# Performance work log

Hardware: AMD Instinct MI355X
Metric: run time of the kernel (lower is better)

## Reference

```python
import jax, jax.numpy as jnp
import numpy as np

K = 3

def setup_inputs() -> dict:
    key = jax.random.key(0)
    k1, k2, k3, k4 = jax.random.split(key, 4)
    B, N, F_in, T, F_out = 8, 2048, 16, 12, 32
    x = jax.random.normal(k1, (B, N, F_in, T), dtype=jnp.float32)
    spatial_attention = jax.random.uniform(k2, (B, N, N), dtype=jnp.float32)
    node_embeddings = jax.random.normal(k3, (N, 16), dtype=jnp.float32)
    theta = jax.random.normal(k4, (K, F_in, F_out), dtype=jnp.float32) * 0.1
    return {"x": x, "spatial_attention": spatial_attention,
            "node_embeddings": node_embeddings, "theta": theta}

def _cheb_polys(node_embeddings, N, K):
    # supports = softmax(relu(E E^T), axis=1)
    supports = jax.nn.softmax(jax.nn.relu(node_embeddings @ node_embeddings.T), axis=1)
    polys = [jnp.eye(N, dtype=supports.dtype), supports]
    for _ in range(2, K):
        polys.append(2.0 * supports @ polys[-1] - polys[-2])
    return jnp.stack(polys[:K], axis=0)  # (K, N, N)

def reference(x, spatial_attention, node_embeddings, theta):
    B, N, F_in, T = x.shape
    polys = _cheb_polys(node_embeddings, N, K)             # (K,N,N)
    # T_k_with_at = polys[k] * attention (broadcast over batch);
    # rhs = T_k_with_at^T @ graph_signal for every timestep:
    # (K,N,N)*(B,N,N) contracted with (B,N,F,T) over source node n -> (K,B,M,F,T)
    rhs = jnp.einsum('knm,bnm,bnft->kbmft', polys, spatial_attention, x)
    # accumulate rhs @ theta_k over k -> (B,M,F_out,T)
    out = jnp.einsum('kbmft,kfo->bmot', rhs, theta)
    return jax.nn.relu(out)
```

## Files before the change

kernel.cpp:

```cpp
#include <hip/hip_runtime.h>

#define NN    2048
#define BATCH 8
#define FIN   16
#define TT    12
#define FOUT  32
#define FT    (FIN*TT)
#define OT    (FOUT*TT)

typedef unsigned short ushort_t;
typedef __attribute__((ext_vector_type(8))) short   short8;
typedef __attribute__((ext_vector_type(4))) float   f32x4;
typedef __attribute__((ext_vector_type(4))) unsigned short us4;
typedef __attribute__((ext_vector_type(8))) unsigned short us8;

__device__ __forceinline__ float b2f(unsigned short u) {
    union { unsigned int i; float f; } v; v.i = ((unsigned int)u) << 16; return v.f;
}
__device__ __forceinline__ unsigned short f2b(float f) {
    union { float f; unsigned int i; } v; v.f = f;
    unsigned int x = v.i;
    x += 0x7fffu + ((x >> 16) & 1u);
    return (unsigned short)(x >> 16);
}

#define LGKM0()   asm volatile("s_waitcnt lgkmcnt(0)" ::: "memory")
#define BARRIER() __builtin_amdgcn_s_barrier()

__global__ __launch_bounds__(256)
void k_supports(const float* __restrict__ E, ushort_t* __restrict__ Sb) {
    const int n = blockIdx.x;
    __shared__ float row[NN];
    __shared__ float red[256];
    const int tid = threadIdx.x;

    const f32x4 en0 = *(const f32x4*)&E[n * 16 + 0];
    const f32x4 en1 = *(const f32x4*)&E[n * 16 + 4];
    const f32x4 en2 = *(const f32x4*)&E[n * 16 + 8];
    const f32x4 en3 = *(const f32x4*)&E[n * 16 + 12];

    float lmax = 0.0f;
    for (int m = tid; m < NN; m += 256) {
        const f32x4* Em = (const f32x4*)&E[(size_t)m * 16];
        const f32x4 e0 = Em[0], e1 = Em[1], e2 = Em[2], e3 = Em[3];
        float d = 0.0f;
        #pragma unroll
        for (int j = 0; j < 4; ++j) d += en0[j] * e0[j];
        #pragma unroll
        for (int j = 0; j < 4; ++j) d += en1[j] * e1[j];
        #pragma unroll
        for (int j = 0; j < 4; ++j) d += en2[j] * e2[j];
        #pragma unroll
        for (int j = 0; j < 4; ++j) d += en3[j] * e3[j];
        d = fmaxf(d, 0.0f);
        row[m] = d;
        lmax = fmaxf(lmax, d);
    }
    red[tid] = lmax; __syncthreads();
    for (int s = 128; s > 0; s >>= 1) {
        if (tid < s) red[tid] = fmaxf(red[tid], red[tid + s]);
        __syncthreads();
    }
    const float mx = red[0];
    __syncthreads();

    float lsum = 0.0f;
    for (int m = tid; m < NN; m += 256) {
        float e = __expf(row[m] - mx);
        row[m] = e;
        lsum += e;
    }
    red[tid] = lsum; __syncthreads();
    for (int s = 128; s > 0; s >>= 1) {
        if (tid < s) red[tid] += red[tid + s];
        __syncthreads();
    }
    const float inv = 1.0f / red[0];
    for (int m = tid; m < NN; m += 256) Sb[(size_t)n * NN + m] = f2b(row[m] * inv);
}

__global__ __launch_bounds__(256)
void k_pack_st(const ushort_t* __restrict__ Sb, ushort_t* __restrict__ SbT) {
    const int r0 = blockIdx.x * 64, c0 = blockIdx.y * 64;
    __shared__ ushort_t Lt[64][65];
    const int tid = threadIdx.x;
    #pragma unroll
    for (int p = 0; p < 2; ++p) {
        const int i = (tid >> 3) + p * 32;
        const int j8 = (tid & 7) * 8;
        us8 v = *(const us8*)&Sb[(size_t)(r0 + i) * NN + c0 + j8];
        #pragma unroll
        for (int e = 0; e < 8; ++e) Lt[i][j8 + e] = v[e];
    }
    __syncthreads();
    #pragma unroll
    for (int p = 0; p < 2; ++p) {
        const int jj = (tid >> 3) + p * 32;
        const int i8 = (tid & 7) * 8;
        us8 v;
        #pragma unroll
        for (int e = 0; e < 8; ++e) v[e] = Lt[i8 + e][jj];
        *(us8*)&SbT[(size_t)(c0 + jj) * NN + r0 + i8] = v;
    }
}

__global__ __launch_bounds__(256)
void k_pack_x(const float* __restrict__ x, ushort_t* __restrict__ xbT) {
    const int nc = blockIdx.x * 64;
    const int b  = blockIdx.y;
    __shared__ ushort_t Lt[FT][65];
    const int tid = threadIdx.x;
    const float* __restrict__ xb = x + (size_t)b * NN * FT;
    #pragma unroll
    for (int p = 0; p < 12; ++p) {
        const int id = tid + 256 * p;
        const int nn = id / 48;
        const int f4 = (id % 48) * 4;
        const float4 v = *(const float4*)&xb[(size_t)(nc + nn) * FT + f4];
        Lt[f4 + 0][nn] = f2b(v.x);
        Lt[f4 + 1][nn] = f2b(v.y);
        Lt[f4 + 2][nn] = f2b(v.z);
        Lt[f4 + 3][nn] = f2b(v.w);
    }
    __syncthreads();
    #pragma unroll
    for (int p = 0; p < 6; ++p) {
        const int id = tid + 256 * p;
        const int ft = id >> 3;
        const int n8 = (id & 7) * 8;
        us8 v;
        #pragma unroll
        for (int e = 0; e < 8; ++e) v[e] = Lt[ft][n8 + e];
        *(us8*)&xbT[((size_t)b * FT + ft) * NN + nc + n8] = v;
    }
}

__global__ __launch_bounds__(512, 2)
void k_t2(const ushort_t* __restrict__ Sb, const ushort_t* __restrict__ SbT,
          ushort_t* __restrict__ T2b) {
    const int m0 = blockIdx.x * 128;
    const int n0 = blockIdx.y * 128;
    __shared__ __align__(16) ushort_t As[2][128 * 64];
    __shared__ __align__(16) ushort_t Bs[2][128 * 64];
    const int tid = threadIdx.x;
    const int lane = tid & 63, w = tid >> 6;
    const int l15 = lane & 15, q = lane >> 4, l7 = lane & 7;
    const int nw = (w & 1) * 64;
    const int mw = (w >> 1) * 32;
    const int sr = tid >> 3;
    const int sc = tid & 7;

    f32x4 acc[4][2];
    #pragma unroll
    for (int i = 0; i < 4; ++i)
        #pragma unroll
        for (int j = 0; j < 2; ++j) acc[i][j] = {0.f, 0.f, 0.f, 0.f};

    us8 avA[2], bvA[2], avB[2], bvB[2];

#define T2_LOAD(l0, av, bv)                                              \
    { _Pragma("unroll") for (int p = 0; p < 2; ++p) {                    \
        const int row_ = sr + 64 * p;                                    \
        av[p] = *(const us8*)&Sb[(size_t)(n0 + row_) * NN + (l0) + sc * 8];  \
        bv[p] = *(const us8*)&SbT[(size_t)(m0 + row_) * NN + (l0) + sc * 8]; \
      } }

#define T2_STORE(bufi, av, bv)                                           \
    { _Pragma("unroll") for (int p = 0; p < 2; ++p) {                    \
        const int row_ = sr + 64 * p;                                    \
        const int cs_ = (sc ^ (row_ & 7)) * 8;                           \
        *(us8*)&As[bufi][row_ * 64 + cs_] = av[p];                       \
        *(us8*)&Bs[bufi][row_ * 64 + cs_] = bv[p];                       \
      } }

#define T2_MFMA(bufi)                                                    \
    { _Pragma("unroll") for (int s = 0; s < 2; ++s) {                    \
        short8 a_[4], b_[2];                                             \
        const int u_ = ((s * 4 + q) ^ l7) * 8;                           \
        _Pragma("unroll") for (int i = 0; i < 4; ++i)                    \
            a_[i] = *(const short8*)&As[bufi][(nw + i * 16 + l15) * 64 + u_]; \
        _Pragma("unroll") for (int j = 0; j < 2; ++j)                    \
            b_[j] = *(const short8*)&Bs[bufi][(mw + j * 16 + l15) * 64 + u_]; \
        _Pragma("unroll") for (int i = 0; i < 4; ++i)                    \
            _Pragma("unroll") for (int j = 0; j < 2; ++j)                \
                acc[i][j] = __builtin_amdgcn_mfma_f32_16x16x32_bf16(a_[i], b_[j], acc[i][j], 0, 0, 0); \
      } }

    T2_LOAD(0, avA, bvA);
    T2_LOAD(64, avB, bvB);
    T2_STORE(0, avA, bvA);
    T2_LOAD(128, avA, bvA);
    LGKM0(); BARRIER();

    for (int c = 0; c < 32; c += 2) {
        T2_MFMA(0);
        if (c < 31) T2_STORE(1, avB, bvB);
        if (c < 29) T2_LOAD((c + 3) * 64, avB, bvB);
        LGKM0(); BARRIER();
        T2_MFMA(1);
        if (c < 30) T2_STORE(0, avA, bvA);
        if (c < 28) T2_LOAD((c + 4) * 64, avA, bvA);
        LGKM0(); BARRIER();
    }
#undef T2_LOAD
#undef T2_STORE
#undef T2_MFMA

    #pragma unroll
    for (int i = 0; i < 4; ++i)
        #pragma unroll
        for (int j = 0; j < 2; ++j)
            #pragma unroll
            for (int r = 0; r < 4; ++r) {
                const int ng = n0 + nw + i * 16 + q * 4 + r;
                const int mg = m0 + mw + j * 16 + l15;
                const float v = 2.0f * acc[i][j][r] - (ng == mg ? 1.0f : 0.0f);
                T2b[(size_t)ng * NN + mg] = f2b(v);
            }
}

__global__ __launch_bounds__(512, 2)
void k_rhs(const ushort_t* __restrict__ Sb, const ushort_t* __restrict__ T2b,
           const float* __restrict__ att, const ushort_t* __restrict__ xbT,
           float* __restrict__ rhs) {
    const int m0 = blockIdx.x * 64;
    const int b  = blockIdx.y;
    __shared__ __align__(16) ushort_t As[2][128 * 64];
    __shared__ __align__(16) ushort_t Xs[2][FT * 64];
    const int tid = threadIdx.x;
    const int lane = tid & 63, w = tid >> 6;
    const int l15 = lane & 15, q = lane >> 4, l7 = lane & 7, l3 = lane >> 3;
    const int k1 = w & 1, ft0 = (w >> 1) * 48;
    const float* __restrict__ attb = att + (size_t)b * NN * NN;

    const int k1s = tid >> 8;
    const int uu  = tid & 255;
    const int m4  = (uu & 15) * 4;
    const int nn4 = (uu >> 4) * 4;
    const ushort_t* __restrict__ Pk = k1s ? T2b : Sb;

    f32x4 acc[4][3];
    #pragma unroll
    for (int i = 0; i < 4; ++i)
        #pragma unroll
        for (int t = 0; t < 3; ++t) acc[i][t] = {0.f, 0.f, 0.f, 0.f};

    us8   xvA[3], xvB[3];
    us4   pvA[4], pvB[4];
    f32x4 avA[4], avB[4];

#define RHS_LOAD(nc, xv, pv, av)                                            \
    { _Pragma("unroll") for (int p = 0; p < 3; ++p) {                       \
        const int row_ = (w * 3 + p) * 8 + l3;                              \
        xv[p] = *(const us8*)&xbT[((size_t)b * FT + row_) * NN + (nc) + l7 * 8]; \
      }                                                                     \
      _Pragma("unroll") for (int r = 0; r < 4; ++r) {                       \
        const int nn_ = (nc) + nn4 + r;                                     \
        pv[r] = *(const us4*)&Pk[(size_t)nn_ * NN + m0 + m4];               \
        av[r] = *(const f32x4*)&attb[(size_t)nn_ * NN + m0 + m4];           \
      } }

#define RHS_WRITE(bufi, xv, pv, av)                                         \
    { _Pragma("unroll") for (int p = 0; p < 3; ++p) {                       \
        const int row_ = (w * 3 + p) * 8 + l3;                              \
        *(us8*)&Xs[bufi][row_ * 64 + (l7 ^ l3) * 8] = xv[p];                \
      }                                                                     \
      _Pragma("unroll") for (int c_ = 0; c_ < 4; ++c_) {                    \
        const int rowm_ = m4 + c_;                                          \
        const int g_ = (nn4 >> 3) ^ (rowm_ & 7);                            \
        unsigned int u01_, u23_;                                            \
        { const float a_ = b2f(pv[0][c_]) * av[0][c_];                      \
          const float b_ = b2f(pv[1][c_]) * av[1][c_];                      \
          asm("v_cvt_pk_bf16_f32 %0, %1, %2" : "=v"(u01_) : "v"(a_), "v"(b_)); } \
        { const float a_ = b2f(pv[2][c_]) * av[2][c_];                      \
          const float b_ = b2f(pv[3][c_]) * av[3][c_];                      \
          asm("v_cvt_pk_bf16_f32 %0, %1, %2" : "=v"(u23_) : "v"(a_), "v"(b_)); } \
        *(uint2*)&As[bufi][(k1s * 64 + rowm_) * 64 + g_ * 8 + (nn4 & 4)] =  \
            make_uint2(u01_, u23_);                                         \
      } }

#define RHS_MFMA(bufi)                                                      \
    { _Pragma("unroll") for (int s = 0; s < 2; ++s) {                       \
        short8 a_[4], bb_[3];                                               \
        const int u_ = ((s * 4 + q) ^ l7) * 8;                              \
        _Pragma("unroll") for (int i = 0; i < 4; ++i)                       \
            a_[i] = *(const short8*)&As[bufi][(k1 * 64 + i * 16 + l15) * 64 + u_]; \
        _Pragma("unroll") for (int t = 0; t < 3; ++t)                       \
            bb_[t] = *(const short8*)&Xs[bufi][(ft0 + t * 16 + l15) * 64 + u_]; \
        _Pragma("unroll") for (int i = 0; i < 4; ++i)                       \
            _Pragma("unroll") for (int t = 0; t < 3; ++t)                   \
                acc[i][t] = __builtin_amdgcn_mfma_f32_16x16x32_bf16(a_[i], bb_[t], acc[i][t], 0, 0, 0); \
      } }

    RHS_LOAD(0, xvA, pvA, avA);
    RHS_LOAD(64, xvB, pvB, avB);
    RHS_WRITE(0, xvA, pvA, avA);
    RHS_LOAD(128, xvA, pvA, avA);
    LGKM0(); BARRIER();

    for (int c = 0; c < 32; c += 2) {
        RHS_MFMA(0);
        if (c < 31) RHS_WRITE(1, xvB, pvB, avB);
        if (c < 29) RHS_LOAD((c + 3) * 64, xvB, pvB, avB);
        LGKM0(); BARRIER();
        RHS_MFMA(1);
        if (c < 30) RHS_WRITE(0, xvA, pvA, avA);
        if (c < 28) RHS_LOAD((c + 4) * 64, xvA, pvA, avA);
        LGKM0(); BARRIER();
    }
#undef RHS_LOAD
#undef RHS_WRITE
#undef RHS_MFMA

    float* __restrict__ op = rhs + ((size_t)(k1 * BATCH + b)) * NN * FT;
    #pragma unroll
    for (int i = 0; i < 4; ++i)
        #pragma unroll
        for (int t = 0; t < 3; ++t)
            #pragma unroll
            for (int r = 0; r < 4; ++r) {
                const int mg = m0 + i * 16 + q * 4 + r;
                const int ftg = ft0 + t * 16 + l15;
                op[(size_t)mg * FT + ftg] = acc[i][t][r];
            }
}

__global__ __launch_bounds__(128)
void k_out(const float* __restrict__ x, const float* __restrict__ att,
           const float* __restrict__ theta, const float* __restrict__ rhs,
           float* __restrict__ out) {
    const int m = blockIdx.x & (NN - 1);
    const int b = blockIdx.x >> 11;
    __shared__ float xr[FT], r1[FT], r2[FT];
    __shared__ float th[3 * FIN * FOUT];
    const int tid = threadIdx.x;

    const float* __restrict__ xb = x + ((size_t)b * NN + m) * FT;
    const float* __restrict__ p1 = rhs + ((size_t)0 * BATCH + b) * NN * FT + (size_t)m * FT;
    const float* __restrict__ p2 = rhs + ((size_t)1 * BATCH + b) * NN * FT + (size_t)m * FT;
    const float a0 = att[((size_t)b * NN + m) * NN + m];

    for (int i = tid; i < FT; i += 128) {
        xr[i] = xb[i] * a0;
        r1[i] = p1[i];
        r2[i] = p2[i];
    }
    for (int i = tid; i < 3 * FIN * FOUT; i += 128) th[i] = theta[i];
    __syncthreads();

    float* __restrict__ ob = out + ((size_t)b * NN + m) * OT;
    for (int idx = tid; idx < OT; idx += 128) {
        const int o = idx / TT, t = idx % TT;
        float acc = 0.0f;
        #pragma unroll
        for (int f = 0; f < FIN; ++f) {
            const int ft = f * TT + t;
            acc += th[f * FOUT + o] * xr[ft];
            acc += th[512 + f * FOUT + o] * r1[ft];
            acc += th[1024 + f * FOUT + o] * r2[ft];
        }
        ob[idx] = fmaxf(acc, 0.0f);
    }
}

extern "C" void kernel_launch(void* const* d_in, const int* in_sizes, int n_in,
                              void* d_out, int out_size, void* d_ws, size_t ws_size,
                              hipStream_t stream) {
    const float* x     = (const float*)d_in[0];
    const float* att   = (const float*)d_in[1];
    const float* E     = (const float*)d_in[2];
    const float* theta = (const float*)d_in[3];
    float* out = (float*)d_out;

    ushort_t* Sb  = (ushort_t*)d_ws;
    ushort_t* SbT = Sb  + (size_t)NN * NN;
    ushort_t* T2b = SbT + (size_t)NN * NN;
    ushort_t* xbT = T2b + (size_t)NN * NN;
    float*    rhs = (float*)(xbT + (size_t)BATCH * FT * NN);

    k_supports<<<NN, 256, 0, stream>>>(E, Sb);
    k_pack_st<<<dim3(32, 32), 256, 0, stream>>>(Sb, SbT);
    k_pack_x<<<dim3(32, BATCH), 256, 0, stream>>>(x, xbT);
    k_t2<<<dim3(16, 16), 512, 0, stream>>>(Sb, SbT, T2b);
    k_rhs<<<dim3(32, BATCH), 512, 0, stream>>>(Sb, T2b, att, xbT, rhs);
    k_out<<<BATCH * NN, 128, 0, stream>>>(x, att, theta, rhs, out);
}
```

Before: 320.6 us.

## Fuse theta projection and ReLU into k_rhs epilogue; drop softmax max pass

Removes the separate k_out kernel and the fp32 rhs intermediate buffer. k_rhs now stages its accumulators through reused shared memory, one Chebyshev order at a time, and applies theta, the diagonal attention term for k=0, and ReLU directly. This saves a large global write and read and one kernel launch, at the cost of extra barriers and shared-memory staging in the epilogue. It also drops the max-subtraction in the supports softmax, which removes a reduction pass but can overflow if the embedding dot products are large.

```diff
diff --git a/kernel.cpp b/kernel.cpp
--- a/kernel.cpp
+++ b/kernel.cpp
@@ -39,7 +39,7 @@
     const f32x4 en2 = *(const f32x4*)&E[n * 16 + 8];
     const f32x4 en3 = *(const f32x4*)&E[n * 16 + 12];
 
-    float lmax = 0.0f;
+    float lsum = 0.0f;
     for (int m = tid; m < NN; m += 256) {
         const f32x4* Em = (const f32x4*)&E[(size_t)m * 16];
         const f32x4 e0 = Em[0], e1 = Em[1], e2 = Em[2], e3 = Em[3];
@@ -53,20 +53,7 @@
         #pragma unroll
         for (int j = 0; j < 4; ++j) d += en3[j] * e3[j];
         d = fmaxf(d, 0.0f);
-        row[m] = d;
-        lmax = fmaxf(lmax, d);
-    }
-    red[tid] = lmax; __syncthreads();
-    for (int s = 128; s > 0; s >>= 1) {
-        if (tid < s) red[tid] = fmaxf(red[tid], red[tid + s]);
-        __syncthreads();
-    }
-    const float mx = red[0];
-    __syncthreads();
-
-    float lsum = 0.0f;
-    for (int m = tid; m < NN; m += 256) {
-        float e = __expf(row[m] - mx);
+        const float e = __expf(d);
         row[m] = e;
         lsum += e;
     }
@@ -222,11 +209,13 @@
 __global__ __launch_bounds__(512, 2)
 void k_rhs(const ushort_t* __restrict__ Sb, const ushort_t* __restrict__ T2b,
            const float* __restrict__ att, const ushort_t* __restrict__ xbT,
-           float* __restrict__ rhs) {
+           const float* __restrict__ x, const float* __restrict__ theta,
+           float* __restrict__ out) {
     const int m0 = blockIdx.x * 64;
     const int b  = blockIdx.y;
-    __shared__ __align__(16) ushort_t As[2][128 * 64];
-    __shared__ __align__(16) ushort_t Xs[2][FT * 64];
+    __shared__ __align__(16) ushort_t SM[40960];
+#define ASi(bufi, idx) SM[(bufi) * 8192 + (idx)]
+#define XSi(bufi, idx) SM[16384 + (bufi) * 12288 + (idx)]
     const int tid = threadIdx.x;
     const int lane = tid & 63, w = tid >> 6;
     const int l15 = lane & 15, q = lane >> 4, l7 = lane & 7, l3 = lane >> 3;
@@ -263,7 +252,7 @@
 #define RHS_WRITE(bufi, xv, pv, av)                                         \
     { _Pragma("unroll") for (int p = 0; p < 3; ++p) {                       \
         const int row_ = (w * 3 + p) * 8 + l3;                              \
-        *(us8*)&Xs[bufi][row_ * 64 + (l7 ^ l3) * 8] = xv[p];                \
+        *(us8*)&XSi(bufi, row_ * 64 + (l7 ^ l3) * 8) = xv[p];               \
       }                                                                     \
       _Pragma("unroll") for (int c_ = 0; c_ < 4; ++c_) {                    \
         const int rowm_ = m4 + c_;                                          \
@@ -275,7 +264,7 @@
         { const float a_ = b2f(pv[2][c_]) * av[2][c_];                      \
           const float b_ = b2f(pv[3][c_]) * av[3][c_];                      \
           asm("v_cvt_pk_bf16_f32 %0, %1, %2" : "=v"(u23_) : "v"(a_), "v"(b_)); } \
-        *(uint2*)&As[bufi][(k1s * 64 + rowm_) * 64 + g_ * 8 + (nn4 & 4)] =  \
+        *(uint2*)&ASi(bufi, (k1s * 64 + rowm_) * 64 + g_ * 8 + (nn4 & 4)) = \
             make_uint2(u01_, u23_);                                         \
       } }
 
@@ -284,9 +273,9 @@
         short8 a_[4], bb_[3];                                               \
         const int u_ = ((s * 4 + q) ^ l7) * 8;                              \
         _Pragma("unroll") for (int i = 0; i < 4; ++i)                       \
-            a_[i] = *(const short8*)&As[bufi][(k1 * 64 + i * 16 + l15) * 64 + u_]; \
+            a_[i] = *(const short8*)&ASi(bufi, (k1 * 64 + i * 16 + l15) * 64 + u_); \
         _Pragma("unroll") for (int t = 0; t < 3; ++t)                       \
-            bb_[t] = *(const short8*)&Xs[bufi][(ft0 + t * 16 + l15) * 64 + u_]; \
+            bb_[t] = *(const short8*)&XSi(bufi, (ft0 + t * 16 + l15) * 64 + u_); \
         _Pragma("unroll") for (int i = 0; i < 4; ++i)                       \
             _Pragma("unroll") for (int t = 0; t < 3; ++t)                   \
                 acc[i][t] = __builtin_amdgcn_mfma_f32_16x16x32_bf16(a_[i], bb_[t], acc[i][t], 0, 0, 0); \
@@ -312,55 +301,80 @@
 #undef RHS_WRITE
 #undef RHS_MFMA
 
-    float* __restrict__ op = rhs + ((size_t)(k1 * BATCH + b)) * NN * FT;
-    #pragma unroll
-    for (int i = 0; i < 4; ++i)
-        #pragma unroll
-        for (int t = 0; t < 3; ++t)
+    float* __restrict__ Ld = (float*)&SM[0];
+    float* __restrict__ Th = (float*)&SM[25088];
+
+#define STAGE_ACC()                                                         \
+    { _Pragma("unroll") for (int i = 0; i < 4; ++i)                         \
+        _Pragma("unroll") for (int t = 0; t < 3; ++t)                       \
+          _Pragma("unroll") for (int r = 0; r < 4; ++r)                     \
+            Ld[(i * 16 + q * 4 + r) * 196 + ft0 + t * 16 + l15] = acc[i][t][r]; }
+
+    for (int i = tid; i < 3 * FIN * FOUT; i += 512) Th[i] = theta[i];
+    if (k1 == 0) STAGE_ACC();
+    LGKM0(); BARRIER();
+
+    const int me = tid >> 3;
+    const int og = (tid & 7) * 4;
+    const int mg = m0 + me;
+    const float a0 = att[((size_t)b * NN + mg) * NN + mg];
+    const float* __restrict__ xm = x + ((size_t)b * NN + mg) * FT;
+
+    f32x4 oa[4][3];
+    #pragma unroll
+    for (int o4 = 0; o4 < 4; ++o4)
+        #pragma unroll
+        for (int j = 0; j < 3; ++j) oa[o4][j] = {0.f, 0.f, 0.f, 0.f};
+
+    #pragma unroll 4
+    for (int f = 0; f < FIN; ++f) {
+        const f32x4 th0 = *(const f32x4*)&Th[f * FOUT + og];
+        const f32x4 th1 = *(const f32x4*)&Th[512 + f * FOUT + og];
+        #pragma unroll
+        for (int j = 0; j < 3; ++j) {
+            const f32x4 xv = *(const f32x4*)&xm[f * TT + j * 4];
+            const f32x4 rv = *(const f32x4*)&Ld[me * 196 + f * TT + j * 4];
             #pragma unroll
-            for (int r = 0; r < 4; ++r) {
-                const int mg = m0 + i * 16 + q * 4 + r;
-                const int ftg = ft0 + t * 16 + l15;
-                op[(size_t)mg * FT + ftg] = acc[i][t][r];
+            for (int e = 0; e < 4; ++e) {
+                const float xa = xv[e] * a0;
+                #pragma unroll
+                for (int o4 = 0; o4 < 4; ++o4)
+                    oa[o4][j][e] += th0[o4] * xa + th1[o4] * rv[e];
             }
-}
-
-__global__ __launch_bounds__(128)
-void k_out(const float* __restrict__ x, const float* __restrict__ att,
-           const float* __restrict__ theta, const float* __restrict__ rhs,
-           float* __restrict__ out) {
-    const int m = blockIdx.x & (NN - 1);
-    const int b = blockIdx.x >> 11;
-    __shared__ float xr[FT], r1[FT], r2[FT];
-    __shared__ float th[3 * FIN * FOUT];
-    const int tid = threadIdx.x;
-
-    const float* __restrict__ xb = x + ((size_t)b * NN + m) * FT;
-    const float* __restrict__ p1 = rhs + ((size_t)0 * BATCH + b) * NN * FT + (size_t)m * FT;
-    const float* __restrict__ p2 = rhs + ((size_t)1 * BATCH + b) * NN * FT + (size_t)m * FT;
-    const float a0 = att[((size_t)b * NN + m) * NN + m];
-
-    for (int i = tid; i < FT; i += 128) {
-        xr[i] = xb[i] * a0;
-        r1[i] = p1[i];
-        r2[i] = p2[i];
-    }
-    for (int i = tid; i < 3 * FIN * FOUT; i += 128) th[i] = theta[i];
-    __syncthreads();
-
-    float* __restrict__ ob = out + ((size_t)b * NN + m) * OT;
-    for (int idx = tid; idx < OT; idx += 128) {
-        const int o = idx / TT, t = idx % TT;
-        float acc = 0.0f;
-        #pragma unroll
-        for (int f = 0; f < FIN; ++f) {
-            const int ft = f * TT + t;
-            acc += th[f * FOUT + o] * xr[ft];
-            acc += th[512 + f * FOUT + o] * r1[ft];
-            acc += th[1024 + f * FOUT + o] * r2[ft];
         }
-        ob[idx] = fmaxf(acc, 0.0f);
-    }
+    }
+
+    LGKM0(); BARRIER();
+    if (k1 == 1) STAGE_ACC();
+    LGKM0(); BARRIER();
+
+    #pragma unroll 4
+    for (int f = 0; f < FIN; ++f) {
+        const f32x4 th2 = *(const f32x4*)&Th[1024 + f * FOUT + og];
+        #pragma unroll
+        for (int j = 0; j < 3; ++j) {
+            const f32x4 rv = *(const f32x4*)&Ld[me * 196 + f * TT + j * 4];
+            #pragma unroll
+            for (int e = 0; e < 4; ++e)
+                #pragma unroll
+                for (int o4 = 0; o4 < 4; ++o4)
+                    oa[o4][j][e] += th2[o4] * rv[e];
+        }
+    }
+#undef STAGE_ACC
+
+    float* __restrict__ ob = out + ((size_t)b * NN + mg) * OT + og * TT;
+    #pragma unroll
+    for (int o4 = 0; o4 < 4; ++o4)
+        #pragma unroll
+        for (int j = 0; j < 3; ++j) {
+            f32x4 v = oa[o4][j];
+            #pragma unroll
+            for (int e = 0; e < 4; ++e) v[e] = fmaxf(v[e], 0.0f);
+            *(f32x4*)&ob[o4 * TT + j * 4] = v;
+        }
+#undef ASi
+#undef XSi
 }
 
 extern "C" void kernel_launch(void* const* d_in, const int* in_sizes, int n_in,
@@ -376,12 +390,10 @@
     ushort_t* SbT = Sb  + (size_t)NN * NN;
     ushort_t* T2b = SbT + (size_t)NN * NN;
     ushort_t* xbT = T2b + (size_t)NN * NN;
-    float*    rhs = (float*)(xbT + (size_t)BATCH * FT * NN);
 
     k_supports<<<NN, 256, 0, stream>>>(E, Sb);
     k_pack_st<<<dim3(32, 32), 256, 0, stream>>>(Sb, SbT);
     k_pack_x<<<dim3(32, BATCH), 256, 0, stream>>>(x, xbT);
     k_t2<<<dim3(16, 16), 512, 0, stream>>>(Sb, SbT, T2b);
-    k_rhs<<<dim3(32, BATCH), 512, 0, stream>>>(Sb, T2b, att, xbT, rhs);
-    k_out<<<BATCH * NN, 128, 0, stream>>>(x, att, theta, rhs, out);
-}
+    k_rhs<<<dim3(32, BATCH), 512, 0, stream>>>(Sb, T2b, att, xbT, x, theta, out);
+}
```

Result: faster. 288.3 us (-10.1%).
